# Kernel tuning notes

Measured on AMD Instinct MI355X. Metric: run time of the kernel, lower is better.

## Reference

```python
import jax, jax.numpy as jnp
import numpy as np

NHEAD, HD, ITERS = 8, 32, 6


def _layernorm(x, g, b, eps=1e-5):
    mu = jnp.mean(x, axis=-1, keepdims=True)
    var = jnp.mean((x - mu) ** 2, axis=-1, keepdims=True)
    return g * (x - mu) / jnp.sqrt(var + eps) + b


def _msa1(x, ax, WQ, bQ, WK, bK, WV, bV, WO, bO):
    # ring (sliding-window, size 3) attention + relay node as 4th key/value
    B, L, H = x.shape
    q = (x @ WQ + bQ).reshape(B, L, NHEAD, HD)
    k = (x @ WK + bK).reshape(B, L, NHEAD, HD)
    ak = (ax @ WK + bK).reshape(B, 1, NHEAD, 1, HD)   # relay key
    av = (ax @ WV + bV).reshape(B, 1, NHEAD, 1, HD)   # relay value
    padk = jnp.pad(k, ((0, 0), (1, 1), (0, 0), (0, 0)))
    wins = jnp.stack([padk[:, t:L + t] for t in range(3)], axis=3)  # [B,L,nh,3,hd]
    ak_b = jnp.broadcast_to(ak, (B, L, NHEAD, 1, HD))
    av_b = jnp.broadcast_to(av, (B, L, NHEAD, 1, HD))
    keys = jnp.concatenate([ak_b, wins], axis=3)   # [B,L,nh,4,hd]
    # NOTE: faithful to source bug: window VALUES come from k (pad_v = F.pad(k,...))
    vals = jnp.concatenate([av_b, wins], axis=3)
    scores = jnp.einsum('blnd,blnkd->blnk', q, keys) / np.sqrt(HD).astype(np.float32)
    alphas = jax.nn.softmax(scores, axis=-1)
    att = jnp.einsum('blnk,blnkd->blnd', alphas, vals).reshape(B, L, NHEAD * HD)
    return att @ WO + bO


def _msa2(x, y, WQ, bQ, WK, bK, WV, bV, WO, bO):
    # relay attends over [relay; nodes]; mask arg is ignored in the original
    B, L1, H = y.shape
    q = (x @ WQ + bQ).reshape(B, NHEAD, HD)
    k = (y @ WK + bK).reshape(B, L1, NHEAD, HD)
    v = (y @ WV + bV).reshape(B, L1, NHEAD, HD)
    scores = jnp.einsum('bnd,blnd->bnl', q, k) / np.sqrt(HD).astype(np.float32)
    alphas = jax.nn.softmax(scores, axis=-1)
    att = jnp.einsum('bnl,blnd->bnd', alphas, v).reshape(B, NHEAD * HD)
    return att @ WO + bO


def setup_inputs() -> dict:
    key = jax.random.key(0)
    ks = jax.random.split(key, 32)
    B, L, H, V, E, I = 32, 512, 256, 32000, 300, 6

    def rn(k, shape, s=0.05):
        return jax.random.normal(k, shape, jnp.float32) * s

    inp = {
        'data': jax.random.randint(ks[0], (B, L), 0, V),
        'emb': rn(ks[1], (V, E), 0.1),
        'emb_fc_W': rn(ks[2], (E, H)),
        'emb_fc_b': jnp.zeros((H,), jnp.float32),
        'pos_emb': rn(ks[3], (1000, H), 0.02),
        'ln_g': jnp.ones((I, H), jnp.float32),
        'ln_b': jnp.zeros((I, H), jnp.float32),
    }
    names = ['r_WQ', 'r_WK', 'r_WV', 'r_WO', 's_WQ', 's_WK', 's_WV', 's_WO']
    for j, n in enumerate(names):
        inp[n] = rn(ks[4 + j], (I, H, H))
        inp[n.replace('W', 'b')] = rn(ks[12 + j], (I, H), 0.01)
    return inp


def reference(data, emb, emb_fc_W, emb_fc_b, pos_emb, ln_g, ln_b,
              r_WQ, r_bQ, r_WK, r_bK, r_WV, r_bV, r_WO, r_bO,
              s_WQ, s_bQ, s_WK, s_bK, s_WV, s_bV, s_WO, s_bO):
    B, L = data.shape
    mask = (data == 1)
    e = emb[data]                                  # [B,L,nemb]
    P = pos_emb[:L][None]                          # [1,L,H]
    x0 = e @ emb_fc_W + emb_fc_b + P               # [B,L,H]
    nodes = x0
    relay = jnp.mean(x0, axis=1)                   # [B,H]
    for i in range(ITERS):
        ax = relay
        n_ln = _layernorm(nodes, ln_g[i], ln_b[i])
        nodes = nodes + jax.nn.leaky_relu(
            _msa1(n_ln, ax, r_WQ[i], r_bQ[i], r_WK[i], r_bK[i],
                  r_WV[i], r_bV[i], r_WO[i], r_bO[i]))
        y = jnp.concatenate([relay[:, None, :], nodes], axis=1)
        relay = jax.nn.leaky_relu(
            _msa2(relay, y, s_WQ[i], s_bQ[i], s_WK[i], s_bK[i],
                  s_WV[i], s_bV[i], s_WO[i], s_bO[i]))
        nodes = jnp.where(mask[:, :, None], 0.0, nodes)
    rep = 0.5 * jnp.max(nodes, axis=1) + 0.5 * relay
    return rep
```

## Files before the change

### kernel.cpp

```cpp
#include <hip/hip_runtime.h>
#include <stdint.h>

typedef __bf16 bf16x8 __attribute__((ext_vector_type(8)));
typedef unsigned short ushort8 __attribute__((ext_vector_type(8)));
typedef float floatx4 __attribute__((ext_vector_type(4)));

__device__ __forceinline__ unsigned short f2b(float f) {
    unsigned int u = __builtin_bit_cast(unsigned int, f);
    u += 0x7fffu + ((u >> 16) & 1u);
    return (unsigned short)(u >> 16);
}
__device__ __forceinline__ float b2f(unsigned short u) {
    union { unsigned int i; float f; } x; x.i = ((unsigned int)u) << 16; return x.f;
}
__device__ __forceinline__ void gl_lds16(const unsigned short* g, unsigned short* l) {
    __builtin_amdgcn_global_load_lds(
        (const __attribute__((address_space(1))) unsigned int*)g,
        (__attribute__((address_space(3))) unsigned int*)l, 16, 0, 0);
}

#define SCALE_QK 0.17677669529663687f

__global__ __launch_bounds__(256) void transpose_many(const float* __restrict__ w0,
                                                      const float* __restrict__ w1,
                                                      const float* __restrict__ w2,
                                                      const float* __restrict__ w3,
                                                      const float* __restrict__ w4,
                                                      const float* __restrict__ wemb,
                                                      unsigned short* __restrict__ out,
                                                      unsigned short* __restrict__ outEmb,
                                                      float* __restrict__ relayAcc) {
    __shared__ float tile[64][65];
    int m = blockIdx.y;
    int tid = threadIdx.x;
    if (m == 30) {
#pragma unroll
        for (int i = 0; i < 20; i++) {
            int e = i * 4096 + blockIdx.x * 256 + tid;
            int n = e / 320, k = e - n * 320;
            outEmb[e] = (k < 300) ? f2b(wemb[k * 256 + n]) : (unsigned short)0;
        }
        if (blockIdx.x == 0) {
#pragma unroll
            for (int j = 0; j < 32; j++) relayAcc[j * 256 + tid] = 0.f;
        }
        return;
    }
    int fam = m / 6, it = m % 6;
    const float* src =
        (fam == 0 ? w0 : fam == 1 ? w1 : fam == 2 ? w2 : fam == 3 ? w3 : w4) + it * 65536;
    unsigned short* dst = out + (size_t)(it * 5 + fam) * 65536;
    int k0 = (blockIdx.x & 3) * 64, n0 = (blockIdx.x >> 2) * 64;
    int rg = tid >> 6, cl = tid & 63;
#pragma unroll
    for (int i = 0; i < 16; i++) {
        int kl = rg * 16 + i;
        tile[kl][cl] = src[(k0 + kl) * 256 + n0 + cl];
    }
    __syncthreads();
#pragma unroll
    for (int i = 0; i < 16; i++) {
        int nl = rg * 16 + i;
        dst[(n0 + nl) * 256 + k0 + cl] = f2b(tile[cl][nl]);
    }
}

__global__ void gather_emb(const int* __restrict__ data,
                           const float* __restrict__ emb,
                           unsigned short* __restrict__ apad) {
    int row = blockIdx.x;
    int tok = data[row];
    const float* er = emb + (size_t)tok * 300;
    for (int c = threadIdx.x; c < 320; c += 256)
        apad[(size_t)row * 320 + c] = (c < 300) ? f2b(er[c]) : (unsigned short)0;
}

template <int EPI, int KDIM, int NC>
__global__ __launch_bounds__(256) void gemm_k(const unsigned short* __restrict__ A,
                                              const unsigned short* __restrict__ Bt,
                                              const float* __restrict__ bias0,
                                              const float* __restrict__ bias1,
                                              float* __restrict__ outF,
                                              unsigned short* __restrict__ outB0,
                                              unsigned short* __restrict__ outB1,
                                              const float* __restrict__ pos,
                                              const int* __restrict__ dmask,
                                              int applyMask,
                                              float* __restrict__ relayAcc) {
    constexpr int G = KDIM / 8;
    __shared__ unsigned short Asm[64 * KDIM];
    __shared__ unsigned short Bsm[64 * KDIM];
    const int tid = threadIdx.x;
    const int wave = tid >> 6, lane = tid & 63;
    const int wm = (wave >> 1) * 32, wn = (wave & 1) * 32;
    const int quad = lane >> 4, l16 = lane & 15;
    const int id = blockIdx.x;
    const int xcd = id & 7, t = id >> 3;
    const int cIdx = t % NC, rhi = t / NC;
    const int rowBase = (rhi * 8 + xcd) * 64, colBase = cIdx * 64;
    {
        const unsigned short* gbA = A + (size_t)(rowBase + wave * 16) * KDIM;
        const unsigned short* gbB = Bt + (size_t)(colBase + wave * 16) * KDIM;
        unsigned short* lbA = Asm + wave * 16 * KDIM;
        unsigned short* lbB = Bsm + wave * 16 * KDIM;
#pragma unroll
        for (int c = 0; c < G / 4; c++) {
            int gi = c * 64 + lane;
            int rl = gi / G, sl = gi - rl * G;
            int sg = sl ^ (rl & 7);
            gl_lds16(gbA + rl * KDIM + sg * 8, lbA + gi * 8);
            gl_lds16(gbB + rl * KDIM + sg * 8, lbB + gi * 8);
        }
    }
    __syncthreads();

    floatx4 acc[2][2] = {};
    const int mr0 = wm + l16, mr1 = wm + 16 + l16;
    const int nr0 = wn + l16, nr1 = wn + 16 + l16;
#pragma unroll
    for (int ks = 0; ks < KDIM / 32; ks++) {
        int g = ks * 4 + quad;
        bf16x8 af0 = __builtin_bit_cast(bf16x8, *(const ushort8*)&Asm[mr0 * KDIM + ((g ^ (mr0 & 7)) * 8)]);
        bf16x8 af1 = __builtin_bit_cast(bf16x8, *(const ushort8*)&Asm[mr1 * KDIM + ((g ^ (mr1 & 7)) * 8)]);
        bf16x8 bf0 = __builtin_bit_cast(bf16x8, *(const ushort8*)&Bsm[nr0 * KDIM + ((g ^ (nr0 & 7)) * 8)]);
        bf16x8 bf1 = __builtin_bit_cast(bf16x8, *(const ushort8*)&Bsm[nr1 * KDIM + ((g ^ (nr1 & 7)) * 8)]);
        acc[0][0] = __builtin_amdgcn_mfma_f32_16x16x32_bf16(af0, bf0, acc[0][0], 0, 0, 0);
        acc[0][1] = __builtin_amdgcn_mfma_f32_16x16x32_bf16(af0, bf1, acc[0][1], 0, 0, 0);
        acc[1][0] = __builtin_amdgcn_mfma_f32_16x16x32_bf16(af1, bf0, acc[1][0], 0, 0, 0);
        acc[1][1] = __builtin_amdgcn_mfma_f32_16x16x32_bf16(af1, bf1, acc[1][1], 0, 0, 0);
    }
    if (EPI == 0) {
        const int group = colBase >> 8;
        const float* bias = group ? bias1 : bias0;
        unsigned short* obf = group ? outB1 : outB0;
        unsigned short* tile = Asm;
        __syncthreads();
#pragma unroll
        for (int tm = 0; tm < 2; tm++) {
#pragma unroll
            for (int tn = 0; tn < 2; tn++) {
                int lcl = wn + tn * 16 + l16;
                float bv = bias[(colBase & 255) + lcl];
#pragma unroll
                for (int r = 0; r < 4; r++) {
                    int rl = wm + tm * 16 + quad * 4 + r;
                    tile[rl * 72 + lcl] = f2b(acc[tm][tn][r] + bv);
                }
            }
        }
        __syncthreads();
#pragma unroll
        for (int j = 0; j < 2; j++) {
            int c = j * 256 + tid;
            int rl = c >> 3, c8 = c & 7;
            ushort8 v = *(const ushort8*)&tile[rl * 72 + c8 * 8];
            *(ushort8*)(obf + (size_t)(rowBase + rl) * 256 + (colBase & 255) + c8 * 8) = v;
        }
    } else {
#pragma unroll
        for (int tm = 0; tm < 2; tm++) {
#pragma unroll
            for (int tn = 0; tn < 2; tn++) {
                int col = colBase + wn + tn * 16 + l16;
                int lc = col & 255;
                float bv = bias0[lc];
                float cs = 0.f;
#pragma unroll
                for (int r = 0; r < 4; r++) {
                    int row = rowBase + wm + tm * 16 + quad * 4 + r;
                    float c = acc[tm][tn][r] + bv;
                    size_t o = (size_t)row * 256 + lc;
                    if (EPI == 1) {
                        float v = c > 0.f ? c : 0.01f * c;
                        float base = outF[o];
                        if (applyMask && dmask[row] == 1) base = 0.f;
                        float rr = base + v;
                        outF[o] = rr;
                        outB0[o] = f2b(rr);
                    } else {
                        float v = c + pos[(row & 511) * 256 + lc];
                        outF[o] = v;
                        cs += v;
                    }
                }
                if (EPI == 2) {
                    cs += __shfl_xor(cs, 16);
                    cs += __shfl_xor(cs, 32);
                    if (quad == 0)
                        atomicAdd(&relayAcc[(rowBase >> 9) * 256 + lc], cs * (1.f / 512.f));
                }
            }
        }
    }
}

__global__ __launch_bounds__(256) void ln_k(const float* __restrict__ nodes,
                                            const float* __restrict__ g,
                                            const float* __restrict__ bb,
                                            unsigned short* __restrict__ out,
                                            const int* __restrict__ dmask,
                                            int applyMask) {
    __shared__ float red[8];
    int row = blockIdx.x, t = threadIdx.x;
    int wv = t >> 6, ln_ = t & 63;
    float x = nodes[(size_t)row * 256 + t];
    if (applyMask && dmask[row] == 1) x = 0.f;
    float s = x;
#pragma unroll
    for (int o = 32; o; o >>= 1) s += __shfl_xor(s, o);
    if (ln_ == 0) red[wv] = s;
    __syncthreads();
    float mu = (red[0] + red[1] + red[2] + red[3]) * (1.f / 256.f);
    float d = x - mu;
    float v = d * d;
#pragma unroll
    for (int o = 32; o; o >>= 1) v += __shfl_xor(v, o);
    if (ln_ == 0) red[4 + wv] = v;
    __syncthreads();
    float var = (red[4] + red[5] + red[6] + red[7]) * (1.f / 256.f);
    float inv = rsqrtf(var + 1e-5f);
    out[(size_t)row * 256 + t] = f2b(g[t] * d * inv + bb[t]);
}

__global__ __launch_bounds__(1024) void relay5(const float* __restrict__ relay,
                       const float* __restrict__ rWK, const float* __restrict__ rbK,
                       const float* __restrict__ rWV, const float* __restrict__ rbV,
                       const float* __restrict__ sWQ, const float* __restrict__ sbQ,
                       const float* __restrict__ sWK, const float* __restrict__ sbK,
                       const float* __restrict__ sWV, const float* __restrict__ sbV,
                       float* __restrict__ AK, float* __restrict__ AV,
                       float* __restrict__ Q2, float* __restrict__ RK2, float* __restrict__ RV2) {
    __shared__ float r[256];
    __shared__ float part[1024];
    int b = blockIdx.x, fam = blockIdx.y, t = threadIdx.x;
    if (t < 256) r[t] = relay[b * 256 + t];
    __syncthreads();
    const float* W; const float* bi; float* o;
    switch (fam) {
        case 0: W = rWK; bi = rbK; o = AK; break;
        case 1: W = rWV; bi = rbV; o = AV; break;
        case 2: W = sWQ; bi = sbQ; o = Q2; break;
        case 3: W = sWK; bi = sbK; o = RK2; break;
        default: W = sWV; bi = sbV; o = RV2; break;
    }
    int col = t & 255, kc = t >> 8;
    float s = 0.f;
    for (int e = kc * 64; e < kc * 64 + 64; e++) s += r[e] * W[e * 256 + col];
    part[t] = s;
    __syncthreads();
    if (kc == 0)
        o[b * 256 + col] = part[col] + part[256 + col] + part[512 + col] + part[768 + col] + bi[col];
}

__global__ __launch_bounds__(256) void attn1_k(const unsigned short* __restrict__ q,
                                               const unsigned short* __restrict__ k,
                                               const float* __restrict__ ak,
                                               const float* __restrict__ av,
                                               unsigned short* __restrict__ att) {
    int tid = threadIdx.x;
    int nb = (blockIdx.x & 7) * 512 + (blockIdx.x >> 3);
    int row = nb * 4 + (tid >> 6);
    int b = row >> 9, l = row & 511;
    int t = tid & 63;
    size_t o = (size_t)row * 256 + t * 4;
    ushort4 z4; z4.x = z4.y = z4.z = z4.w = 0;
    ushort4 q4 = *(const ushort4*)(q + o);
    ushort4 k04 = *(const ushort4*)(k + o);
    ushort4 km4 = (l > 0) ? *(const ushort4*)(k + o - 256) : z4;
    ushort4 kp4 = (l < 511) ? *(const ushort4*)(k + o + 256) : z4;
    float4 akv = *(const float4*)(ak + b * 256 + t * 4);
    float4 avv = *(const float4*)(av + b * 256 + t * 4);
    float qv0 = b2f(q4.x), qv1 = b2f(q4.y), qv2 = b2f(q4.z), qv3 = b2f(q4.w);
    float k00 = b2f(k04.x), k01 = b2f(k04.y), k02 = b2f(k04.z), k03 = b2f(k04.w);
    float km0 = b2f(km4.x), km1 = b2f(km4.y), km2 = b2f(km4.z), km3 = b2f(km4.w);
    float kp0 = b2f(kp4.x), kp1 = b2f(kp4.y), kp2 = b2f(kp4.z), kp3 = b2f(kp4.w);
    float s0 = qv0 * akv.x + qv1 * akv.y + qv2 * akv.z + qv3 * akv.w;
    float s1 = qv0 * km0 + qv1 * km1 + qv2 * km2 + qv3 * km3;
    float s2 = qv0 * k00 + qv1 * k01 + qv2 * k02 + qv3 * k03;
    float s3 = qv0 * kp0 + qv1 * kp1 + qv2 * kp2 + qv3 * kp3;
#pragma unroll
    for (int off = 4; off; off >>= 1) {
        s0 += __shfl_xor(s0, off);
        s1 += __shfl_xor(s1, off);
        s2 += __shfl_xor(s2, off);
        s3 += __shfl_xor(s3, off);
    }
    s0 *= SCALE_QK; s1 *= SCALE_QK; s2 *= SCALE_QK; s3 *= SCALE_QK;
    float m = fmaxf(fmaxf(s0, s1), fmaxf(s2, s3));
    float e0 = __expf(s0 - m), e1 = __expf(s1 - m), e2 = __expf(s2 - m), e3 = __expf(s3 - m);
    float iZ = 1.f / (e0 + e1 + e2 + e3);
    ushort4 r4;
    r4.x = f2b((e0 * avv.x + e1 * km0 + e2 * k00 + e3 * kp0) * iZ);
    r4.y = f2b((e0 * avv.y + e1 * km1 + e2 * k01 + e3 * kp1) * iZ);
    r4.z = f2b((e0 * avv.z + e1 * km2 + e2 * k02 + e3 * kp2) * iZ);
    r4.w = f2b((e0 * avv.w + e1 * km3 + e2 * k03 + e3 * kp3) * iZ);
    *(ushort4*)(att + o) = r4;
}

__global__ __launch_bounds__(512) void attn2_k(const float* __restrict__ q2,
                                               const unsigned short* __restrict__ k2,
                                               const unsigned short* __restrict__ v2,
                                               const float* __restrict__ rk2,
                                               const float* __restrict__ rv2,
                                               float* __restrict__ att2) {
    __shared__ float sc[513];
    __shared__ float qs[32];
    __shared__ float red[16];
    __shared__ float red2[512];
    int bn = blockIdx.x;
    int b = bn >> 3, n = bn & 7;
    int t = threadIdx.x;
    if (t < 32) qs[t] = q2[b * 256 + n * 32 + t];
    __syncthreads();
    float lmax = -1e30f;
    for (int li = t; li < 513; li += 512) {
        float d = 0.f;
        if (li == 0) {
            const float* kr = rk2 + b * 256 + n * 32;
#pragma unroll 8
            for (int j = 0; j < 32; j++) d += qs[j] * kr[j];
        } else {
            const unsigned short* kr = k2 + ((size_t)(b * 512 + li - 1) * 256 + n * 32);
#pragma unroll 8
            for (int j = 0; j < 32; j++) d += qs[j] * b2f(kr[j]);
        }
        d *= SCALE_QK;
        sc[li] = d;
        lmax = fmaxf(lmax, d);
    }
#pragma unroll
    for (int o = 32; o; o >>= 1) lmax = fmaxf(lmax, __shfl_xor(lmax, o));
    if ((t & 63) == 0) red[t >> 6] = lmax;
    __syncthreads();
    float m = red[0];
#pragma unroll
    for (int i = 1; i < 8; i++) m = fmaxf(m, red[i]);
    float lsum = 0.f;
    for (int li = t; li < 513; li += 512) {
        float e = __expf(sc[li] - m);
        sc[li] = e;
        lsum += e;
    }
#pragma unroll
    for (int o = 32; o; o >>= 1) lsum += __shfl_xor(lsum, o);
    if ((t & 63) == 0) red[8 + (t >> 6)] = lsum;
    __syncthreads();
    float Z = red[8];
#pragma unroll
    for (int i = 9; i < 16; i++) Z += red[i];
    int d_ = t & 31, g_ = t >> 5;
    float acc = 0.f;
    for (int li = g_; li < 513; li += 16) {
        if (li == 0) {
            acc += sc[0] * rv2[b * 256 + n * 32 + d_];
        } else {
            acc += sc[li] * b2f(v2[(size_t)(b * 512 + li - 1) * 256 + n * 32 + d_]);
        }
    }
    red2[t] = acc;
    __syncthreads();
    if (t < 32) {
        float s = 0.f;
#pragma unroll
        for (int g = 0; g < 16; g++) s += red2[g * 32 + t];
        att2[b * 256 + n * 32 + t] = s / Z;
    }
}

__global__ __launch_bounds__(1024) void relay_out2(const float* __restrict__ att2,
                           const float* __restrict__ WO, const float* __restrict__ bO,
                           float* __restrict__ relay) {
    __shared__ float r[256];
    __shared__ float part[1024];
    int b = blockIdx.x, t = threadIdx.x;
    if (t < 256) r[t] = att2[b * 256 + t];
    __syncthreads();
    int col = t & 255, kc = t >> 8;
    float s = 0.f;
    for (int e = kc * 64; e < kc * 64 + 64; e++) s += r[e] * WO[e * 256 + col];
    part[t] = s;
    __syncthreads();
    if (kc == 0) {
        float tot = part[col] + part[256 + col] + part[512 + col] + part[768 + col] + bO[col];
        relay[b * 256 + col] = tot > 0.f ? tot : 0.01f * tot;
    }
}

__global__ void rep_part(const float* __restrict__ nodes, const int* __restrict__ dmask,
                         float* __restrict__ part) {
    int b = blockIdx.x, c = blockIdx.y, h = threadIdx.x;
    const float* p = nodes + ((size_t)b * 512 + c * 32) * 256 + h;
    const int* dd = dmask + b * 512 + c * 32;
    float m = -1e30f;
    for (int l = 0; l < 32; l++) {
        float v = (dd[l] == 1) ? 0.f : p[l * 256];
        m = fmaxf(m, v);
    }
    part[(b * 16 + c) * 256 + h] = m;
}
__global__ void rep_comb(const float* __restrict__ part, const float* __restrict__ relay,
                         float* __restrict__ out) {
    int b = blockIdx.x, h = threadIdx.x;
    float m = -1e30f;
    for (int c = 0; c < 16; c++) m = fmaxf(m, part[(b * 16 + c) * 256 + h]);
    out[b * 256 + h] = 0.5f * m + 0.5f * relay[b * 256 + h];
}

extern "C" void kernel_launch(void* const* d_in, const int* in_sizes, int n_in,
                              void* d_out, int out_size, void* d_ws, size_t ws_size,
                              hipStream_t stream) {
    const int* data = (const int*)d_in[0];
    const float* emb = (const float*)d_in[1];
    const float* emb_fc_W = (const float*)d_in[2];
    const float* emb_fc_b = (const float*)d_in[3];
    const float* pos_emb = (const float*)d_in[4];
    const float* ln_g = (const float*)d_in[5];
    const float* ln_b = (const float*)d_in[6];
    const float* r_WQ = (const float*)d_in[7];
    const float* r_bQ = (const float*)d_in[8];
    const float* r_WK = (const float*)d_in[9];
    const float* r_bK = (const float*)d_in[10];
    const float* r_WV = (const float*)d_in[11];
    const float* r_bV = (const float*)d_in[12];
    const float* r_WO = (const float*)d_in[13];
    const float* r_bO = (const float*)d_in[14];
    const float* s_WQ = (const float*)d_in[15];
    const float* s_bQ = (const float*)d_in[16];
    const float* s_WK = (const float*)d_in[17];
    const float* s_bK = (const float*)d_in[18];
    const float* s_WV = (const float*)d_in[19];
    const float* s_bV = (const float*)d_in[20];
    const float* s_WO = (const float*)d_in[21];
    const float* s_bO = (const float*)d_in[22];

    char* w = (char*)d_ws;
    size_t off = 0;
    auto alloc = [&](size_t bytes) -> char* {
        char* p = w + off;
        off += (bytes + 255) & ~(size_t)255;
        return p;
    };
    float* RELAY = (float*)alloc(8192 * 4);
    float* AK = (float*)alloc(8192 * 4);
    float* AV = (float*)alloc(8192 * 4);
    float* Q2 = (float*)alloc(8192 * 4);
    float* RK2 = (float*)alloc(8192 * 4);
    float* RV2 = (float*)alloc(8192 * 4);
    float* ATT2 = (float*)alloc(8192 * 4);
    float* PART = (float*)alloc((size_t)32 * 16 * 256 * 4);
    unsigned short* WTE = (unsigned short*)alloc((size_t)256 * 320 * 2);
    unsigned short* WT = (unsigned short*)alloc((size_t)30 * 65536 * 2);
    float* NODES = (float*)alloc((size_t)16384 * 256 * 4);
    unsigned short* NLN = (unsigned short*)alloc((size_t)16384 * 256 * 2);
    unsigned short* Qb = (unsigned short*)alloc((size_t)16384 * 256 * 2);
    unsigned short* Kb16 = (unsigned short*)alloc((size_t)16384 * 256 * 2);
    unsigned short* NBF = (unsigned short*)alloc((size_t)16384 * 320 * 2);
    unsigned short* AEMB = NBF;
    unsigned short* ATT = NLN;
    unsigned short* K2b = Qb;
    unsigned short* V2b = Kb16;

    transpose_many<<<dim3(16, 31), 256, 0, stream>>>(r_WQ, r_WK, r_WO, s_WK, s_WV,
                                                     emb_fc_W, WT, WTE, RELAY);
    gather_emb<<<16384, 256, 0, stream>>>(data, emb, AEMB);
    gemm_k<2, 320, 4><<<1024, 256, 0, stream>>>(AEMB, WTE, emb_fc_b, nullptr,
                                                NODES, nullptr, nullptr, pos_emb,
                                                nullptr, 0, RELAY);

    for (int i = 0; i < 6; i++) {
        const unsigned short* wQK = WT + (size_t)(i * 5 + 0) * 65536;
        const unsigned short* wO = WT + (size_t)(i * 5 + 2) * 65536;
        const unsigned short* wKV2 = WT + (size_t)(i * 5 + 3) * 65536;

        ln_k<<<16384, 256, 0, stream>>>(NODES, ln_g + i * 256, ln_b + i * 256, NLN, data, i > 0);
        gemm_k<0, 256, 8><<<2048, 256, 0, stream>>>(NLN, wQK, r_bQ + i * 256, r_bK + i * 256,
                                                    nullptr, Qb, Kb16, nullptr, nullptr, 0,
                                                    nullptr);
        relay5<<<dim3(32, 5), 1024, 0, stream>>>(RELAY,
                                                 r_WK + (size_t)i * 65536, r_bK + i * 256,
                                                 r_WV + (size_t)i * 65536, r_bV + i * 256,
                                                 s_WQ + (size_t)i * 65536, s_bQ + i * 256,
                                                 s_WK + (size_t)i * 65536, s_bK + i * 256,
                                                 s_WV + (size_t)i * 65536, s_bV + i * 256,
                                                 AK, AV, Q2, RK2, RV2);
        attn1_k<<<4096, 256, 0, stream>>>(Qb, Kb16, AK, AV, ATT);
        gemm_k<1, 256, 4><<<1024, 256, 0, stream>>>(ATT, wO, r_bO + i * 256, nullptr,
                                                    NODES, NBF, nullptr, nullptr, data, i > 0,
                                                    nullptr);
        gemm_k<0, 256, 8><<<2048, 256, 0, stream>>>(NBF, wKV2, s_bK + i * 256, s_bV + i * 256,
                                                    nullptr, K2b, V2b, nullptr, nullptr, 0,
                                                    nullptr);
        attn2_k<<<256, 512, 0, stream>>>(Q2, K2b, V2b, RK2, RV2, ATT2);
        relay_out2<<<32, 1024, 0, stream>>>(ATT2, s_WO + (size_t)i * 65536, s_bO + i * 256, RELAY);
    }
    rep_part<<<dim3(32, 16), 256, 0, stream>>>(NODES, data, PART);
    rep_comb<<<32, 256, 0, stream>>>(PART, RELAY, (float*)d_out);
}
```

Before: 745.8 us.

## Fuse per-iteration kernels into a cooperative persistent megakernel with grid syncs

Replaces the per-iteration chain of separate launches (layernorm, QK gemm, relay projections, ring attention, output gemm, KV gemm, relay attention, relay output) with one cooperative persistent kernel of 512 blocks. Work is distributed as tasks, and grid.sync() separates the stages. The relay projections are overlapped with layernorm by giving them to spare blocks, and layernorm is rewritten as a one-wave-per-row single-pass variance. The aim is to remove launch overhead and inter-kernel gaps, at the cost of grid-wide barriers, lower occupancy (shared LDS sized for gemm tiles), and a serial 256-wide relay matvec per block. A multi-launch fallback is kept.

```diff
diff --git a/kernel.cpp b/kernel.cpp
--- a/kernel.cpp
+++ b/kernel.cpp
@@ -1,5 +1,8 @@
 #include <hip/hip_runtime.h>
+#include <hip/hip_cooperative_groups.h>
 #include <stdint.h>
+
+namespace cg = cooperative_groups;
 
 typedef __bf16 bf16x8 __attribute__((ext_vector_type(8)));
 typedef unsigned short ushort8 __attribute__((ext_vector_type(8)));
@@ -75,19 +78,13 @@
         apad[(size_t)row * 320 + c] = (c < 300) ? f2b(er[c]) : (unsigned short)0;
 }
 
-template <int EPI, int KDIM, int NC>
-__global__ __launch_bounds__(256) void gemm_k(const unsigned short* __restrict__ A,
-                                              const unsigned short* __restrict__ Bt,
-                                              const float* __restrict__ bias0,
-                                              const float* __restrict__ bias1,
-                                              float* __restrict__ outF,
-                                              unsigned short* __restrict__ outB0,
-                                              unsigned short* __restrict__ outB1,
-                                              const float* __restrict__ pos,
-                                              const int* __restrict__ dmask,
-                                              int applyMask,
-                                              float* __restrict__ relayAcc) {
-    constexpr int G = KDIM / 8;
+__global__ __launch_bounds__(256) void gemm_emb(const unsigned short* __restrict__ A,
+                                                const unsigned short* __restrict__ Bt,
+                                                const float* __restrict__ bias0,
+                                                float* __restrict__ outF,
+                                                const float* __restrict__ pos,
+                                                float* __restrict__ relayAcc) {
+    constexpr int KDIM = 320, G = KDIM / 8, NC = 4;
     __shared__ unsigned short Asm[64 * KDIM];
     __shared__ unsigned short Bsm[64 * KDIM];
     const int tid = threadIdx.x;
@@ -113,7 +110,6 @@
         }
     }
     __syncthreads();
-
     floatx4 acc[2][2] = {};
     const int mr0 = wm + l16, mr1 = wm + 16 + l16;
     const int nr0 = wn + l16, nr1 = wn + 16 + l16;
@@ -129,6 +125,95 @@
         acc[1][0] = __builtin_amdgcn_mfma_f32_16x16x32_bf16(af1, bf0, acc[1][0], 0, 0, 0);
         acc[1][1] = __builtin_amdgcn_mfma_f32_16x16x32_bf16(af1, bf1, acc[1][1], 0, 0, 0);
     }
+#pragma unroll
+    for (int tm = 0; tm < 2; tm++) {
+#pragma unroll
+        for (int tn = 0; tn < 2; tn++) {
+            int col = colBase + wn + tn * 16 + l16;
+            int lc = col & 255;
+            float bv = bias0[lc];
+            float cs = 0.f;
+#pragma unroll
+            for (int r = 0; r < 4; r++) {
+                int row = rowBase + wm + tm * 16 + quad * 4 + r;
+                float v = acc[tm][tn][r] + bv + pos[(row & 511) * 256 + lc];
+                outF[(size_t)row * 256 + lc] = v;
+                cs += v;
+            }
+            cs += __shfl_xor(cs, 16);
+            cs += __shfl_xor(cs, 32);
+            if (quad == 0)
+                atomicAdd(&relayAcc[(rowBase >> 9) * 256 + lc], cs * (1.f / 512.f));
+        }
+    }
+}
+
+struct MA {
+    const int* data;
+    const float* ln_g; const float* ln_b;
+    const unsigned short* WT;
+    const float* r_bQ; const float* r_bK; const float* r_bO;
+    const float* r_WK; const float* r_WV; const float* r_bV;
+    const float* s_WQ; const float* s_bQ;
+    const float* s_WK; const float* s_bK;
+    const float* s_WV; const float* s_bV;
+    const float* s_WO; const float* s_bO;
+    float* NODES; float* RELAY;
+    float* AK; float* AV; float* Q2; float* RK2; float* RV2; float* ATT2;
+    float* PART; float* outp;
+    unsigned short* NLN; unsigned short* Qb; unsigned short* Kb16; unsigned short* NBF;
+};
+
+template <int EPI, int NC>
+__device__ void gemm_tile(const MA& a, int task,
+                          const unsigned short* __restrict__ A,
+                          const unsigned short* __restrict__ Bt,
+                          const float* __restrict__ bias0,
+                          const float* __restrict__ bias1,
+                          float* __restrict__ outF,
+                          unsigned short* __restrict__ outB0,
+                          unsigned short* __restrict__ outB1,
+                          int applyMask,
+                          unsigned short* Asm, unsigned short* Bsm) {
+    constexpr int KDIM = 256;
+    const int tid = threadIdx.x;
+    const int wave = tid >> 6, lane = tid & 63;
+    const int wm = (wave >> 1) * 32, wn = (wave & 1) * 32;
+    const int quad = lane >> 4, l16 = lane & 15;
+    const int xcd = task & 7, t2 = task >> 3;
+    const int cIdx = t2 % NC, rhi = t2 / NC;
+    const int rowBase = (rhi * 8 + xcd) * 64, colBase = cIdx * 64;
+    __syncthreads();
+    {
+        const unsigned short* gbA = A + (size_t)(rowBase + wave * 16) * KDIM;
+        const unsigned short* gbB = Bt + (size_t)(colBase + wave * 16) * KDIM;
+        unsigned short* lbA = Asm + wave * 16 * KDIM;
+        unsigned short* lbB = Bsm + wave * 16 * KDIM;
+#pragma unroll
+        for (int c = 0; c < 8; c++) {
+            int gi = c * 64 + lane;
+            int rl = gi >> 5, sl = gi & 31;
+            int sg = sl ^ (rl & 7);
+            gl_lds16(gbA + rl * KDIM + sg * 8, lbA + gi * 8);
+            gl_lds16(gbB + rl * KDIM + sg * 8, lbB + gi * 8);
+        }
+    }
+    __syncthreads();
+    floatx4 acc[2][2] = {};
+    const int mr0 = wm + l16, mr1 = wm + 16 + l16;
+    const int nr0 = wn + l16, nr1 = wn + 16 + l16;
+#pragma unroll
+    for (int ks = 0; ks < 8; ks++) {
+        int g = ks * 4 + quad;
+        bf16x8 af0 = __builtin_bit_cast(bf16x8, *(const ushort8*)&Asm[mr0 * KDIM + ((g ^ (mr0 & 7)) * 8)]);
+        bf16x8 af1 = __builtin_bit_cast(bf16x8, *(const ushort8*)&Asm[mr1 * KDIM + ((g ^ (mr1 & 7)) * 8)]);
+        bf16x8 bf0 = __builtin_bit_cast(bf16x8, *(const ushort8*)&Bsm[nr0 * KDIM + ((g ^ (nr0 & 7)) * 8)]);
+        bf16x8 bf1 = __builtin_bit_cast(bf16x8, *(const ushort8*)&Bsm[nr1 * KDIM + ((g ^ (nr1 & 7)) * 8)]);
+        acc[0][0] = __builtin_amdgcn_mfma_f32_16x16x32_bf16(af0, bf0, acc[0][0], 0, 0, 0);
+        acc[0][1] = __builtin_amdgcn_mfma_f32_16x16x32_bf16(af0, bf1, acc[0][1], 0, 0, 0);
+        acc[1][0] = __builtin_amdgcn_mfma_f32_16x16x32_bf16(af1, bf0, acc[1][0], 0, 0, 0);
+        acc[1][1] = __builtin_amdgcn_mfma_f32_16x16x32_bf16(af1, bf1, acc[1][1], 0, 0, 0);
+    }
     if (EPI == 0) {
         const int group = colBase >> 8;
         const float* bias = group ? bias1 : bias0;
@@ -162,114 +247,106 @@
 #pragma unroll
             for (int tn = 0; tn < 2; tn++) {
                 int col = colBase + wn + tn * 16 + l16;
-                int lc = col & 255;
-                float bv = bias0[lc];
-                float cs = 0.f;
+                float bv = bias0[col];
 #pragma unroll
                 for (int r = 0; r < 4; r++) {
                     int row = rowBase + wm + tm * 16 + quad * 4 + r;
                     float c = acc[tm][tn][r] + bv;
-                    size_t o = (size_t)row * 256 + lc;
-                    if (EPI == 1) {
-                        float v = c > 0.f ? c : 0.01f * c;
-                        float base = outF[o];
-                        if (applyMask && dmask[row] == 1) base = 0.f;
-                        float rr = base + v;
-                        outF[o] = rr;
-                        outB0[o] = f2b(rr);
-                    } else {
-                        float v = c + pos[(row & 511) * 256 + lc];
-                        outF[o] = v;
-                        cs += v;
-                    }
-                }
-                if (EPI == 2) {
-                    cs += __shfl_xor(cs, 16);
-                    cs += __shfl_xor(cs, 32);
-                    if (quad == 0)
-                        atomicAdd(&relayAcc[(rowBase >> 9) * 256 + lc], cs * (1.f / 512.f));
+                    size_t o = (size_t)row * 256 + col;
+                    float v = c > 0.f ? c : 0.01f * c;
+                    float base = outF[o];
+                    if (applyMask && a.data[row] == 1) base = 0.f;
+                    float rr = base + v;
+                    outF[o] = rr;
+                    outB0[o] = f2b(rr);
                 }
             }
         }
     }
 }
 
-__global__ __launch_bounds__(256) void ln_k(const float* __restrict__ nodes,
-                                            const float* __restrict__ g,
-                                            const float* __restrict__ bb,
-                                            unsigned short* __restrict__ out,
-                                            const int* __restrict__ dmask,
-                                            int applyMask) {
-    __shared__ float red[8];
-    int row = blockIdx.x, t = threadIdx.x;
-    int wv = t >> 6, ln_ = t & 63;
-    float x = nodes[(size_t)row * 256 + t];
-    if (applyMask && dmask[row] == 1) x = 0.f;
-    float s = x;
-#pragma unroll
-    for (int o = 32; o; o >>= 1) s += __shfl_xor(s, o);
-    if (ln_ == 0) red[wv] = s;
-    __syncthreads();
-    float mu = (red[0] + red[1] + red[2] + red[3]) * (1.f / 256.f);
-    float d = x - mu;
-    float v = d * d;
-#pragma unroll
-    for (int o = 32; o; o >>= 1) v += __shfl_xor(v, o);
-    if (ln_ == 0) red[4 + wv] = v;
-    __syncthreads();
-    float var = (red[4] + red[5] + red[6] + red[7]) * (1.f / 256.f);
-    float inv = rsqrtf(var + 1e-5f);
-    out[(size_t)row * 256 + t] = f2b(g[t] * d * inv + bb[t]);
-}
-
-__global__ __launch_bounds__(1024) void relay5(const float* __restrict__ relay,
-                       const float* __restrict__ rWK, const float* __restrict__ rbK,
-                       const float* __restrict__ rWV, const float* __restrict__ rbV,
-                       const float* __restrict__ sWQ, const float* __restrict__ sbQ,
-                       const float* __restrict__ sWK, const float* __restrict__ sbK,
-                       const float* __restrict__ sWV, const float* __restrict__ sbV,
-                       float* __restrict__ AK, float* __restrict__ AV,
-                       float* __restrict__ Q2, float* __restrict__ RK2, float* __restrict__ RV2) {
-    __shared__ float r[256];
-    __shared__ float part[1024];
-    int b = blockIdx.x, fam = blockIdx.y, t = threadIdx.x;
-    if (t < 256) r[t] = relay[b * 256 + t];
-    __syncthreads();
-    const float* W; const float* bi; float* o;
-    switch (fam) {
-        case 0: W = rWK; bi = rbK; o = AK; break;
-        case 1: W = rWV; bi = rbV; o = AV; break;
-        case 2: W = sWQ; bi = sbQ; o = Q2; break;
-        case 3: W = sWK; bi = sbK; o = RK2; break;
-        default: W = sWV; bi = sbV; o = RV2; break;
-    }
-    int col = t & 255, kc = t >> 8;
+__device__ void ln_rows(const MA& a, int it, int applyMask, int nBlocks) {
+    int wave = threadIdx.x >> 6, lane = threadIdx.x & 63;
+    int gw = blockIdx.x * 4 + wave;
+    const float* g = a.ln_g + it * 256;
+    const float* bb = a.ln_b + it * 256;
+    for (int row = gw; row < 16384; row += nBlocks * 4) {
+        float4 x = *(const float4*)(a.NODES + (size_t)row * 256 + lane * 4);
+        if (applyMask && a.data[row] == 1) { x.x = 0.f; x.y = 0.f; x.z = 0.f; x.w = 0.f; }
+        float s = x.x + x.y + x.z + x.w;
+        float q = x.x * x.x + x.y * x.y + x.z * x.z + x.w * x.w;
+#pragma unroll
+        for (int o = 32; o; o >>= 1) { s += __shfl_xor(s, o); q += __shfl_xor(q, o); }
+        float mu = s * (1.f / 256.f);
+        float var = q * (1.f / 256.f) - mu * mu;
+        float inv = rsqrtf(fmaxf(var, 0.f) + 1e-5f);
+        float4 gv = *(const float4*)(g + lane * 4);
+        float4 bv = *(const float4*)(bb + lane * 4);
+        ushort4 r4;
+        r4.x = f2b(gv.x * (x.x - mu) * inv + bv.x);
+        r4.y = f2b(gv.y * (x.y - mu) * inv + bv.y);
+        r4.z = f2b(gv.z * (x.z - mu) * inv + bv.z);
+        r4.w = f2b(gv.w * (x.w - mu) * inv + bv.w);
+        *(ushort4*)(a.NLN + (size_t)row * 256 + lane * 4) = r4;
+    }
+}
+
+__device__ void relay_fams(const MA& a, int b, int j, const float* rs) {
+    int t = threadIdx.x;
+    const float* Ws[5] = {a.r_WK + (size_t)j * 65536, a.r_WV + (size_t)j * 65536,
+                          a.s_WQ + (size_t)j * 65536, a.s_WK + (size_t)j * 65536,
+                          a.s_WV + (size_t)j * 65536};
+    const float* bs[5] = {a.r_bK + j * 256, a.r_bV + j * 256, a.s_bQ + j * 256,
+                          a.s_bK + j * 256, a.s_bV + j * 256};
+    float* os[5] = {a.AK, a.AV, a.Q2, a.RK2, a.RV2};
+#pragma unroll
+    for (int f = 0; f < 5; f++) {
+        const float* W = Ws[f];
+        float s = 0.f;
+#pragma unroll 8
+        for (int e = 0; e < 256; e++) s += rs[e] * W[e * 256 + t];
+        os[f][b * 256 + t] = s + bs[f][t];
+    }
+}
+
+__device__ void relay5_block(const MA& a, int b, float* rs) {
+    int t = threadIdx.x;
+    __syncthreads();
+    rs[t] = a.RELAY[b * 256 + t];
+    __syncthreads();
+    relay_fams(a, b, 0, rs);
+}
+
+__device__ void relayZ_block(const MA& a, int b, int i, bool last, float* rs, float* rr) {
+    int t = threadIdx.x;
+    __syncthreads();
+    rr[t] = a.ATT2[b * 256 + t];
+    __syncthreads();
+    const float* WO = a.s_WO + (size_t)i * 65536;
     float s = 0.f;
-    for (int e = kc * 64; e < kc * 64 + 64; e++) s += r[e] * W[e * 256 + col];
-    part[t] = s;
-    __syncthreads();
-    if (kc == 0)
-        o[b * 256 + col] = part[col] + part[256 + col] + part[512 + col] + part[768 + col] + bi[col];
-}
-
-__global__ __launch_bounds__(256) void attn1_k(const unsigned short* __restrict__ q,
-                                               const unsigned short* __restrict__ k,
-                                               const float* __restrict__ ak,
-                                               const float* __restrict__ av,
-                                               unsigned short* __restrict__ att) {
+#pragma unroll 8
+    for (int e = 0; e < 256; e++) s += rr[e] * WO[e * 256 + t];
+    s += a.s_bO[i * 256 + t];
+    s = s > 0.f ? s : 0.01f * s;
+    a.RELAY[b * 256 + t] = s;
+    rs[t] = s;
+    __syncthreads();
+    if (!last) relay_fams(a, b, i + 1, rs);
+}
+
+__device__ void attn1_task(const MA& a, int nb) {
     int tid = threadIdx.x;
-    int nb = (blockIdx.x & 7) * 512 + (blockIdx.x >> 3);
     int row = nb * 4 + (tid >> 6);
     int b = row >> 9, l = row & 511;
     int t = tid & 63;
     size_t o = (size_t)row * 256 + t * 4;
     ushort4 z4; z4.x = z4.y = z4.z = z4.w = 0;
-    ushort4 q4 = *(const ushort4*)(q + o);
-    ushort4 k04 = *(const ushort4*)(k + o);
-    ushort4 km4 = (l > 0) ? *(const ushort4*)(k + o - 256) : z4;
-    ushort4 kp4 = (l < 511) ? *(const ushort4*)(k + o + 256) : z4;
-    float4 akv = *(const float4*)(ak + b * 256 + t * 4);
-    float4 avv = *(const float4*)(av + b * 256 + t * 4);
+    ushort4 q4 = *(const ushort4*)(a.Qb + o);
+    ushort4 k04 = *(const ushort4*)(a.Kb16 + o);
+    ushort4 km4 = (l > 0) ? *(const ushort4*)(a.Kb16 + o - 256) : z4;
+    ushort4 kp4 = (l < 511) ? *(const ushort4*)(a.Kb16 + o + 256) : z4;
+    float4 akv = *(const float4*)(a.AK + b * 256 + t * 4);
+    float4 avv = *(const float4*)(a.AV + b * 256 + t * 4);
     float qv0 = b2f(q4.x), qv1 = b2f(q4.y), qv2 = b2f(q4.z), qv3 = b2f(q4.w);
     float k00 = b2f(k04.x), k01 = b2f(k04.y), k02 = b2f(k04.z), k03 = b2f(k04.w);
     float km0 = b2f(km4.x), km1 = b2f(km4.y), km2 = b2f(km4.z), km3 = b2f(km4.w);
@@ -294,33 +371,24 @@
     r4.y = f2b((e0 * avv.y + e1 * km1 + e2 * k01 + e3 * kp1) * iZ);
     r4.z = f2b((e0 * avv.z + e1 * km2 + e2 * k02 + e3 * kp2) * iZ);
     r4.w = f2b((e0 * avv.w + e1 * km3 + e2 * k03 + e3 * kp3) * iZ);
-    *(ushort4*)(att + o) = r4;
-}
-
-__global__ __launch_bounds__(512) void attn2_k(const float* __restrict__ q2,
-                                               const unsigned short* __restrict__ k2,
-                                               const unsigned short* __restrict__ v2,
-                                               const float* __restrict__ rk2,
-                                               const float* __restrict__ rv2,
-                                               float* __restrict__ att2) {
-    __shared__ float sc[513];
-    __shared__ float qs[32];
-    __shared__ float red[16];
-    __shared__ float red2[512];
-    int bn = blockIdx.x;
+    *(ushort4*)(a.NLN + o) = r4;
+}
+
+__device__ void attn2_task(const MA& a, int bn, float* sc, float* qs, float* red, float* red2) {
     int b = bn >> 3, n = bn & 7;
     int t = threadIdx.x;
-    if (t < 32) qs[t] = q2[b * 256 + n * 32 + t];
+    __syncthreads();
+    if (t < 32) qs[t] = a.Q2[b * 256 + n * 32 + t];
     __syncthreads();
     float lmax = -1e30f;
-    for (int li = t; li < 513; li += 512) {
+    for (int li = t; li < 513; li += 256) {
         float d = 0.f;
         if (li == 0) {
-            const float* kr = rk2 + b * 256 + n * 32;
+            const float* kr = a.RK2 + b * 256 + n * 32;
 #pragma unroll 8
             for (int j = 0; j < 32; j++) d += qs[j] * kr[j];
         } else {
-            const unsigned short* kr = k2 + ((size_t)(b * 512 + li - 1) * 256 + n * 32);
+            const unsigned short* kr = a.Qb + ((size_t)(b * 512 + li - 1) * 256 + n * 32);
 #pragma unroll 8
             for (int j = 0; j < 32; j++) d += qs[j] * b2f(kr[j]);
         }
@@ -332,11 +400,9 @@
     for (int o = 32; o; o >>= 1) lmax = fmaxf(lmax, __shfl_xor(lmax, o));
     if ((t & 63) == 0) red[t >> 6] = lmax;
     __syncthreads();
-    float m = red[0];
-#pragma unroll
-    for (int i = 1; i < 8; i++) m = fmaxf(m, red[i]);
+    float m = fmaxf(fmaxf(red[0], red[1]), fmaxf(red[2], red[3]));
     float lsum = 0.f;
-    for (int li = t; li < 513; li += 512) {
+    for (int li = t; li < 513; li += 256) {
         float e = __expf(sc[li] - m);
         sc[li] = e;
         lsum += e;
@@ -345,16 +411,14 @@
     for (int o = 32; o; o >>= 1) lsum += __shfl_xor(lsum, o);
     if ((t & 63) == 0) red[8 + (t >> 6)] = lsum;
     __syncthreads();
-    float Z = red[8];
-#pragma unroll
-    for (int i = 9; i < 16; i++) Z += red[i];
+    float Z = red[8] + red[9] + red[10] + red[11];
     int d_ = t & 31, g_ = t >> 5;
     float acc = 0.f;
-    for (int li = g_; li < 513; li += 16) {
+    for (int li = g_; li < 513; li += 8) {
         if (li == 0) {
-            acc += sc[0] * rv2[b * 256 + n * 32 + d_];
+            acc += sc[0] * a.RV2[b * 256 + n * 32 + d_];
         } else {
-            acc += sc[li] * b2f(v2[(size_t)(b * 512 + li - 1) * 256 + n * 32 + d_]);
+            acc += sc[li] * b2f(a.Kb16[(size_t)(b * 512 + li - 1) * 256 + n * 32 + d_]);
         }
     }
     red2[t] = acc;
@@ -362,49 +426,121 @@
     if (t < 32) {
         float s = 0.f;
 #pragma unroll
-        for (int g = 0; g < 16; g++) s += red2[g * 32 + t];
-        att2[b * 256 + n * 32 + t] = s / Z;
-    }
-}
-
-__global__ __launch_bounds__(1024) void relay_out2(const float* __restrict__ att2,
-                           const float* __restrict__ WO, const float* __restrict__ bO,
-                           float* __restrict__ relay) {
-    __shared__ float r[256];
-    __shared__ float part[1024];
-    int b = blockIdx.x, t = threadIdx.x;
-    if (t < 256) r[t] = att2[b * 256 + t];
-    __syncthreads();
-    int col = t & 255, kc = t >> 8;
-    float s = 0.f;
-    for (int e = kc * 64; e < kc * 64 + 64; e++) s += r[e] * WO[e * 256 + col];
-    part[t] = s;
-    __syncthreads();
-    if (kc == 0) {
-        float tot = part[col] + part[256 + col] + part[512 + col] + part[768 + col] + bO[col];
-        relay[b * 256 + col] = tot > 0.f ? tot : 0.01f * tot;
-    }
-}
-
-__global__ void rep_part(const float* __restrict__ nodes, const int* __restrict__ dmask,
-                         float* __restrict__ part) {
-    int b = blockIdx.x, c = blockIdx.y, h = threadIdx.x;
-    const float* p = nodes + ((size_t)b * 512 + c * 32) * 256 + h;
-    const int* dd = dmask + b * 512 + c * 32;
+        for (int g = 0; g < 8; g++) s += red2[g * 32 + t];
+        a.ATT2[b * 256 + n * 32 + t] = s / Z;
+    }
+}
+
+__device__ void rep_part_dev(const MA& a, int b, int c) {
+    int h = threadIdx.x;
+    const float* p = a.NODES + ((size_t)b * 512 + c * 32) * 256 + h;
+    const int* dd = a.data + b * 512 + c * 32;
     float m = -1e30f;
     for (int l = 0; l < 32; l++) {
         float v = (dd[l] == 1) ? 0.f : p[l * 256];
         m = fmaxf(m, v);
     }
-    part[(b * 16 + c) * 256 + h] = m;
-}
-__global__ void rep_comb(const float* __restrict__ part, const float* __restrict__ relay,
-                         float* __restrict__ out) {
-    int b = blockIdx.x, h = threadIdx.x;
+    a.PART[(b * 16 + c) * 256 + h] = m;
+}
+__device__ void rep_comb_dev(const MA& a, int b) {
+    int h = threadIdx.x;
     float m = -1e30f;
-    for (int c = 0; c < 16; c++) m = fmaxf(m, part[(b * 16 + c) * 256 + h]);
-    out[b * 256 + h] = 0.5f * m + 0.5f * relay[b * 256 + h];
-}
+#pragma unroll
+    for (int c = 0; c < 16; c++) m = fmaxf(m, a.PART[(b * 16 + c) * 256 + h]);
+    a.outp[b * 256 + h] = 0.5f * m + 0.5f * a.RELAY[b * 256 + h];
+}
+
+__global__ __launch_bounds__(256, 2) void megak(MA a) {
+    cg::grid_group grid = cg::this_grid();
+    __shared__ unsigned short AsmS[64 * 256];
+    __shared__ unsigned short BsmS[64 * 256];
+    float* pool = (float*)BsmS;
+    float* rsArr = pool;
+    float* rrArr = pool + 256;
+    float* sc = pool + 512;
+    float* qs = pool + 1025;
+    float* red16 = pool + 1057;
+    float* red2 = pool + 1073;
+    const int blk = blockIdx.x;
+    constexpr int NLNB = 480;
+
+    if (blk < NLNB) ln_rows(a, 0, 0, NLNB);
+    else relay5_block(a, blk - NLNB, rsArr);
+    grid.sync();
+
+    for (int i = 0; i < 6; i++) {
+        const unsigned short* wQK = a.WT + (size_t)(i * 5 + 0) * 65536;
+        const unsigned short* wO = a.WT + (size_t)(i * 5 + 2) * 65536;
+        const unsigned short* wKV2 = a.WT + (size_t)(i * 5 + 3) * 65536;
+        for (int tsk = blk; tsk < 2048; tsk += 512)
+            gemm_tile<0, 8>(a, tsk, a.NLN, wQK, a.r_bQ + i * 256, a.r_bK + i * 256,
+                            nullptr, a.Qb, a.Kb16, 0, AsmS, BsmS);
+        grid.sync();
+        for (int tsk = blk; tsk < 4096; tsk += 512) attn1_task(a, tsk);
+        grid.sync();
+        for (int tsk = blk; tsk < 1024; tsk += 512)
+            gemm_tile<1, 4>(a, tsk, a.NLN, wO, a.r_bO + i * 256, nullptr,
+                            a.NODES, a.NBF, nullptr, i > 0, AsmS, BsmS);
+        grid.sync();
+        for (int tsk = blk; tsk < 2048; tsk += 512)
+            gemm_tile<0, 8>(a, tsk, a.NBF, wKV2, a.s_bK + i * 256, a.s_bV + i * 256,
+                            nullptr, a.Qb, a.Kb16, 0, AsmS, BsmS);
+        grid.sync();
+        if (blk < 256) attn2_task(a, blk, sc, qs, red16, red2);
+        grid.sync();
+        if (blk >= NLNB) relayZ_block(a, blk - NLNB, i, i == 5, rsArr, rrArr);
+        else if (i < 5) ln_rows(a, i + 1, 1, NLNB);
+        grid.sync();
+    }
+    rep_part_dev(a, blk >> 4, blk & 15);
+    grid.sync();
+    if (blk < 32) rep_comb_dev(a, blk);
+}
+
+template <int EPI, int NC>
+__global__ __launch_bounds__(256) void gemm_k(MA a,
+                                              const unsigned short* __restrict__ A,
+                                              const unsigned short* __restrict__ Bt,
+                                              const float* __restrict__ bias0,
+                                              const float* __restrict__ bias1,
+                                              float* __restrict__ outF,
+                                              unsigned short* __restrict__ outB0,
+                                              unsigned short* __restrict__ outB1,
+                                              int applyMask) {
+    __shared__ unsigned short Asm[64 * 256];
+    __shared__ unsigned short Bsm[64 * 256];
+    gemm_tile<EPI, NC>(a, blockIdx.x, A, Bt, bias0, bias1, outF, outB0, outB1, applyMask, Asm, Bsm);
+}
+
+__global__ __launch_bounds__(256) void ln_k(MA a, int it, int applyMask) {
+    ln_rows(a, it, applyMask, gridDim.x);
+}
+
+__global__ __launch_bounds__(256) void relay5_k(MA a) {
+    __shared__ float rs[256];
+    relay5_block(a, blockIdx.x, rs);
+}
+
+__global__ __launch_bounds__(256) void relayZ_k(MA a, int i, int last) {
+    __shared__ float rs[256];
+    __shared__ float rr[256];
+    relayZ_block(a, blockIdx.x, i, last != 0, rs, rr);
+}
+
+__global__ __launch_bounds__(256) void attn1_kk(MA a) {
+    attn1_task(a, blockIdx.x);
+}
+
+__global__ __launch_bounds__(256) void attn2_kk(MA a) {
+    __shared__ float sc[513];
+    __shared__ float qs[32];
+    __shared__ float red16[16];
+    __shared__ float red2[256];
+    attn2_task(a, blockIdx.x, sc, qs, red16, red2);
+}
+
+__global__ void rep_part_k(MA a) { rep_part_dev(a, blockIdx.x, blockIdx.y); }
+__global__ void rep_comb_k(MA a) { rep_comb_dev(a, blockIdx.x); }
 
 extern "C" void kernel_launch(void* const* d_in, const int* in_sizes, int n_in,
                               void* d_out, int out_size, void* d_ws, size_t ws_size,
@@ -456,43 +592,54 @@
     unsigned short* Kb16 = (unsigned short*)alloc((size_t)16384 * 256 * 2);
     unsigned short* NBF = (unsigned short*)alloc((size_t)16384 * 320 * 2);
     unsigned short* AEMB = NBF;
-    unsigned short* ATT = NLN;
-    unsigned short* K2b = Qb;
-    unsigned short* V2b = Kb16;
 
     transpose_many<<<dim3(16, 31), 256, 0, stream>>>(r_WQ, r_WK, r_WO, s_WK, s_WV,
                                                      emb_fc_W, WT, WTE, RELAY);
     gather_emb<<<16384, 256, 0, stream>>>(data, emb, AEMB);
-    gemm_k<2, 320, 4><<<1024, 256, 0, stream>>>(AEMB, WTE, emb_fc_b, nullptr,
-                                                NODES, nullptr, nullptr, pos_emb,
-                                                nullptr, 0, RELAY);
-
-    for (int i = 0; i < 6; i++) {
-        const unsigned short* wQK = WT + (size_t)(i * 5 + 0) * 65536;
-        const unsigned short* wO = WT + (size_t)(i * 5 + 2) * 65536;
-        const unsigned short* wKV2 = WT + (size_t)(i * 5 + 3) * 65536;
-
-        ln_k<<<16384, 256, 0, stream>>>(NODES, ln_g + i * 256, ln_b + i * 256, NLN, data, i > 0);
-        gemm_k<0, 256, 8><<<2048, 256, 0, stream>>>(NLN, wQK, r_bQ + i * 256, r_bK + i * 256,
-                                                    nullptr, Qb, Kb16, nullptr, nullptr, 0,
-                                                    nullptr);
-        relay5<<<dim3(32, 5), 1024, 0, stream>>>(RELAY,
-                                                 r_WK + (size_t)i * 65536, r_bK + i * 256,
-                                                 r_WV + (size_t)i * 65536, r_bV + i * 256,
-                                                 s_WQ + (size_t)i * 65536, s_bQ + i * 256,
-                                                 s_WK + (size_t)i * 65536, s_bK + i * 256,
-                                                 s_WV + (size_t)i * 65536, s_bV + i * 256,
-                                                 AK, AV, Q2, RK2, RV2);
-        attn1_k<<<4096, 256, 0, stream>>>(Qb, Kb16, AK, AV, ATT);
-        gemm_k<1, 256, 4><<<1024, 256, 0, stream>>>(ATT, wO, r_bO + i * 256, nullptr,
-                                                    NODES, NBF, nullptr, nullptr, data, i > 0,
-                                                    nullptr);
-        gemm_k<0, 256, 8><<<2048, 256, 0, stream>>>(NBF, wKV2, s_bK + i * 256, s_bV + i * 256,
-                                                    nullptr, K2b, V2b, nullptr, nullptr, 0,
-                                                    nullptr);
-        attn2_k<<<256, 512, 0, stream>>>(Q2, K2b, V2b, RK2, RV2, ATT2);
-        relay_out2<<<32, 1024, 0, stream>>>(ATT2, s_WO + (size_t)i * 65536, s_bO + i * 256, RELAY);
-    }
-    rep_part<<<dim3(32, 16), 256, 0, stream>>>(NODES, data, PART);
-    rep_comb<<<32, 256, 0, stream>>>(PART, RELAY, (float*)d_out);
-}
+    gemm_emb<<<1024, 256, 0, stream>>>(AEMB, WTE, emb_fc_b, NODES, pos_emb, RELAY);
+
+    MA ha;
+    ha.data = data; ha.ln_g = ln_g; ha.ln_b = ln_b; ha.WT = WT;
+    ha.r_bQ = r_bQ; ha.r_bK = r_bK; ha.r_bO = r_bO;
+    ha.r_WK = r_WK; ha.r_WV = r_WV; ha.r_bV = r_bV;
+    ha.s_WQ = s_WQ; ha.s_bQ = s_bQ;
+    ha.s_WK = s_WK; ha.s_bK = s_bK;
+    ha.s_WV = s_WV; ha.s_bV = s_bV;
+    ha.s_WO = s_WO; ha.s_bO = s_bO;
+    ha.NODES = NODES; ha.RELAY = RELAY;
+    ha.AK = AK; ha.AV = AV; ha.Q2 = Q2; ha.RK2 = RK2; ha.RV2 = RV2; ha.ATT2 = ATT2;
+    ha.PART = PART; ha.outp = (float*)d_out;
+    ha.NLN = NLN; ha.Qb = Qb; ha.Kb16 = Kb16; ha.NBF = NBF;
+
+    int dev = 0;
+    hipGetDevice(&dev);
+    int coopAttr = 0;
+    hipDeviceGetAttribute(&coopAttr, hipDeviceAttributeCooperativeLaunch, dev);
+    int maxBlocksPerCU = 0;
+    hipOccupancyMaxActiveBlocksPerMultiprocessor(&maxBlocksPerCU, (const void*)megak, 256, 0);
+
+    if (coopAttr && maxBlocksPerCU >= 2) {
+        void* kargs[] = {(void*)&ha};
+        hipLaunchCooperativeKernel((const void*)megak, dim3(512), dim3(256), kargs, 0, stream);
+    } else {
+        ln_k<<<480, 256, 0, stream>>>(ha, 0, 0);
+        relay5_k<<<32, 256, 0, stream>>>(ha);
+        for (int i = 0; i < 6; i++) {
+            const unsigned short* wQK = WT + (size_t)(i * 5 + 0) * 65536;
+            const unsigned short* wO = WT + (size_t)(i * 5 + 2) * 65536;
+            const unsigned short* wKV2 = WT + (size_t)(i * 5 + 3) * 65536;
+            gemm_k<0, 8><<<2048, 256, 0, stream>>>(ha, NLN, wQK, r_bQ + i * 256, r_bK + i * 256,
+                                                   nullptr, Qb, Kb16, 0);
+            attn1_kk<<<4096, 256, 0, stream>>>(ha);
+            gemm_k<1, 4><<<1024, 256, 0, stream>>>(ha, NLN, wO, r_bO + i * 256, nullptr,
+                                                   NODES, NBF, nullptr, i > 0);
+            gemm_k<0, 8><<<2048, 256, 0, stream>>>(ha, NBF, wKV2, s_bK + i * 256, s_bV + i * 256,
+                                                   nullptr, Qb, Kb16, 0);
+            attn2_kk<<<256, 256, 0, stream>>>(ha);
+            relayZ_k<<<32, 256, 0, stream>>>(ha, i, i == 5 ? 1 : 0);
+            if (i < 5) ln_k<<<480, 256, 0, stream>>>(ha, i + 1, 1);
+        }
+        rep_part_k<<<dim3(32, 16), 256, 0, stream>>>(ha);
+        rep_comb_k<<<32, 256, 0, stream>>>(ha);
+    }
+}
```

Result: slower. 1.061 ms (+42.2%).
